# Kernel tuning notes

Measured on AMD Instinct MI355X. Metric: run time of the kernel, lower is better.

## Reference

```python
import jax, jax.numpy as jnp
import numpy as np

INPUT_SIZE = 128
HIDDEN_SIZE = 512
OUTPUT_SIZE = 128
NUM_LAYERS = 2
BATCH = 256
SEQ_LEN = 512

def _xavier(key, shape):
    fan_out, fan_in = shape
    limit = jnp.sqrt(6.0 / (fan_in + fan_out))
    return jax.random.uniform(key, shape, jnp.float32, -limit, limit)

def setup_inputs() -> dict:
    key = jax.random.key(0)
    ks = jax.random.split(key, 8)
    x = jax.random.normal(ks[0], (BATCH, SEQ_LEN, INPUT_SIZE), jnp.float32)
    hidden = jnp.zeros((NUM_LAYERS, BATCH, HIDDEN_SIZE), jnp.float32)
    W_ih0 = _xavier(ks[1], (HIDDEN_SIZE, INPUT_SIZE))
    W_hh0 = _xavier(ks[2], (HIDDEN_SIZE, HIDDEN_SIZE))
    W_ih1 = _xavier(ks[3], (HIDDEN_SIZE, HIDDEN_SIZE))
    W_hh1 = _xavier(ks[4], (HIDDEN_SIZE, HIDDEN_SIZE))
    b_ih0 = jnp.zeros((HIDDEN_SIZE,), jnp.float32)
    b_hh0 = jnp.zeros((HIDDEN_SIZE,), jnp.float32)
    b_ih1 = jnp.zeros((HIDDEN_SIZE,), jnp.float32)
    b_hh1 = jnp.zeros((HIDDEN_SIZE,), jnp.float32)
    fc_W = _xavier(ks[5], (OUTPUT_SIZE, HIDDEN_SIZE))
    fc_b = jnp.zeros((OUTPUT_SIZE,), jnp.float32)
    return {"x": x, "hidden": hidden,
            "W_ih0": W_ih0, "b_ih0": b_ih0, "W_hh0": W_hh0, "b_hh0": b_hh0,
            "W_ih1": W_ih1, "b_ih1": b_ih1, "W_hh1": W_hh1, "b_hh1": b_hh1,
            "fc_W": fc_W, "fc_b": fc_b}

def _run_layer(seq_tbi, h0, W_ih, b_ih, W_hh, b_hh):
    # seq_tbi: [T, B, I]; h0: [B, H]
    # Precompute input projection for all timesteps (one big GEMM).
    xin = jnp.einsum('tbi,hi->tbh', seq_tbi, W_ih) + b_ih + b_hh  # [T, B, H]
    def step(h, xt):
        h = jnp.tanh(xt + h @ W_hh.T)
        return h, h
    h_last, outs = jax.lax.scan(step, h0, xin)
    return h_last, outs  # outs: [T, B, H]

def reference(x, hidden, W_ih0, b_ih0, W_hh0, b_hh0, W_ih1, b_ih1, W_hh1, b_hh1, fc_W, fc_b):
    seq = jnp.transpose(x, (1, 0, 2))  # [T, B, I]
    h0_last, out0 = _run_layer(seq, hidden[0], W_ih0, b_ih0, W_hh0, b_hh0)
    h1_last, out1 = _run_layer(out0, hidden[1], W_ih1, b_ih1, W_hh1, b_hh1)
    new_hidden = jnp.stack([h0_last, h1_last], axis=0)  # [L, B, H]
    last_hidden = out1[-1]  # [B, H]
    output = last_hidden @ fc_W.T + fc_b  # [B, O]
    return output, new_hidden
```

## Files before the change

kernel.cpp:

```cpp
#include <hip/hip_runtime.h>

#define NB 256
#define NT 512
#define NI 128
#define NH 512
#define NO 128
#define NGRP 16
#define RPG 16
#define BPG 8

typedef __attribute__((ext_vector_type(8))) __bf16 bf16x8;
typedef __attribute__((ext_vector_type(4))) float  f32x4;
typedef unsigned long long u64;

#define MFMA16(a,b,c) __builtin_amdgcn_mfma_f32_16x16x32_bf16((a),(b),(c),0,0,0)

#define XSZ   (RPG*NI*2)
#define HSZ   (RPG*NH*2)
#define XOFF  0
#define H0OFF (2*XSZ)
#define H1OFF (H0OFF + HSZ)
#define SMEM_BYTES (H1OFF + HSZ)

#define SLABU   2048
#define TAGBASE 131072

__device__ __forceinline__ float fast_tanh(float x){
  x = fminf(15.f, fmaxf(-15.f, x));
  float e = __expf(2.f * x);
  return 1.f - 2.f / (e + 1.f);
}

__device__ __forceinline__ bf16x8 cvt8(float4 a, float4 b){
  bf16x8 r;
  r[0]=(__bf16)a.x; r[1]=(__bf16)a.y; r[2]=(__bf16)a.z; r[3]=(__bf16)a.w;
  r[4]=(__bf16)b.x; r[5]=(__bf16)b.y; r[6]=(__bf16)b.z; r[7]=(__bf16)b.w;
  return r;
}

__device__ __forceinline__ bf16x8 loadWfrag(const float* __restrict__ W, int ldk, int row, int k0){
  const float4* p = (const float4*)(W + (size_t)row * ldk + k0);
  return cvt8(p[0], p[1]);
}

__device__ __forceinline__ void st_u64(u64* p, u64 v){
  __hip_atomic_store(p, v, __ATOMIC_RELAXED, __HIP_MEMORY_SCOPE_AGENT);
}
__device__ __forceinline__ u64 ld_u64(const u64* p){
  return __hip_atomic_load(p, __ATOMIC_RELAXED, __HIP_MEMORY_SCOPE_AGENT);
}

__device__ __forceinline__ u64 pack4bf(f32x4 v){
  union { __bf16 h[4]; u64 u; } un;
  un.h[0]=(__bf16)v[0]; un.h[1]=(__bf16)v[1]; un.h[2]=(__bf16)v[2]; un.h[3]=(__bf16)v[3];
  return un.u;
}

__device__ __forceinline__ unsigned cksum(unsigned tick, u64 d){
  return tick + (unsigned)d + (unsigned)(d >> 32);
}

__device__ __forceinline__ u64* slab(u64* b, int l, int p, int g){
  return b + ((size_t)(((l << 1) | p) * NGRP + g)) * SLABU;
}

__global__ __launch_bounds__(256, 1)
void rnn_persistent(const float* __restrict__ x,
                    const float* __restrict__ hid,
                    const float* __restrict__ Wih0, const float* __restrict__ bih0,
                    const float* __restrict__ Whh0, const float* __restrict__ bhh0,
                    const float* __restrict__ Wih1, const float* __restrict__ bih1,
                    const float* __restrict__ Whh1, const float* __restrict__ bhh1,
                    const float* __restrict__ fcW,  const float* __restrict__ fcb,
                    float* __restrict__ out,
                    u64* __restrict__ ex)
{
  __shared__ __align__(16) char smem[SMEM_BYTES];

  const int tid  = threadIdx.x;
  const int lane = tid & 63;
  const int wv   = tid >> 6;
  const int lr   = lane & 15;
  const int lq   = lane >> 4;

  const int bq  = blockIdx.x;
  const int j   = (bq >> 3) & 7;
  const int g   = (bq & 7) + 8 * (bq >> 6);
  const int cb  = j * 64 + wv * 16;
  const int row0 = g * RPG;
  const int myq  = j * 16 + wv * 4 + lq;

  u64* const dat = ex;
  u64* const tag = ex + TAGBASE;

  bf16x8 wih0[4], whh0[16], wih1[16], whh1[16];
#pragma unroll
  for (int kt = 0; kt < 4;  ++kt) wih0[kt] = loadWfrag(Wih0, NI, cb + lr, kt*32 + lq*8);
#pragma unroll
  for (int kt = 0; kt < 16; ++kt) whh0[kt] = loadWfrag(Whh0, NH, cb + lr, kt*32 + lq*8);
#pragma unroll
  for (int kt = 0; kt < 16; ++kt) wih1[kt] = loadWfrag(Wih1, NH, cb + lr, kt*32 + lq*8);
#pragma unroll
  for (int kt = 0; kt < 16; ++kt) whh1[kt] = loadWfrag(Whh1, NH, cb + lr, kt*32 + lq*8);

  const f32x4 bias0 = *(const f32x4*)(bih0 + cb + lq*4) + *(const f32x4*)(bhh0 + cb + lq*4);
  const f32x4 bias1 = *(const f32x4*)(bih1 + cb + lq*4) + *(const f32x4*)(bhh1 + cb + lq*4);

  {
    int r = tid >> 4, i0 = (tid & 15) * 8;
    const float4* xp = (const float4*)(x + ((size_t)(row0 + r) * NT + 0) * NI + i0);
    bf16x8 v = cvt8(xp[0], xp[1]);
    int o = r * 256 + i0 * 2;
    *(bf16x8*)(smem + XOFF + (o ^ ((r & 7) << 4))) = v;
  }
#pragma unroll
  for (int it = 0; it < 4; ++it) {
    int e = it * 2048 + tid * 8;
    int r = e >> 9, c = e & 511;
    int o = r * 1024 + c * 2;
    const float4* hp0 = (const float4*)(hid + (size_t)(row0 + r) * NH + c);
    *(bf16x8*)(smem + H0OFF + (o ^ ((r & 7) << 4))) = cvt8(hp0[0], hp0[1]);
    const float4* hp1 = (const float4*)(hid + (size_t)NB * NH + (size_t)(row0 + r) * NH + c);
    *(bf16x8*)(smem + H1OFF + (o ^ ((r & 7) << 4))) = cvt8(hp1[0], hp1[1]);
  }
  __syncthreads();

#define HFRAG(base, kt) (*(const bf16x8*)((base) + lr * 1024 + (((kt) * 64 + lq * 16) ^ ((lr & 7) << 4))))

#define INGEST(V, D, T, TICK)                                                        \
  for (;;) {                                                                         \
    u64 tg_[8];                                                                      \
    _Pragma("unroll") for (int i_ = 0; i_ < 8; ++i_) V[i_]  = ld_u64((D) + i_*256 + tid); \
    _Pragma("unroll") for (int i_ = 0; i_ < 8; ++i_) tg_[i_] = ld_u64((T) + i_*256 + tid); \
    bool ok_ = true;                                                                 \
    _Pragma("unroll") for (int i_ = 0; i_ < 8; ++i_)                                 \
      ok_ &= ((unsigned)tg_[i_] == cksum((TICK), V[i_]));                            \
    if (ok_) break;                                                                  \
  }

  for (int t = 0; t <= NT; ++t) {
    const char* xA  = smem + XOFF + (t & 1) * XSZ;
    char* h0L = smem + H0OFF;
    char* h1L = smem + H1OFF;
    const bool do0 = (t < NT), do1 = (t > 0);
    const unsigned tick = (unsigned)(t + 1);

    u64* D0 = slab(dat, 0, t & 1, g);        u64* T0 = slab(tag, 0, t & 1, g);
    u64* D1 = slab(dat, 1, (t + 1) & 1, g);  u64* T1 = slab(tag, 1, (t + 1) & 1, g);

    if (do0) {
      f32x4 a0={0.f,0.f,0.f,0.f}, a1={0.f,0.f,0.f,0.f};
#pragma unroll
      for (int kt = 0; kt < 4; ++kt) {
        bf16x8 a = *(const bf16x8*)(xA + lr * 256 + ((kt * 64 + lq * 16) ^ ((lr & 7) << 4)));
        a0 = MFMA16(wih0[kt], a, a0);
      }
#pragma unroll
      for (int kt = 0; kt < 16; ++kt) {
        bf16x8 a = HFRAG(h0L, kt);
        if (kt & 1) a1 = MFMA16(whh0[kt], a, a1); else a0 = MFMA16(whh0[kt], a, a0);
      }
      f32x4 s = a0 + a1 + bias0;
      f32x4 h; h[0]=fast_tanh(s[0]); h[1]=fast_tanh(s[1]); h[2]=fast_tanh(s[2]); h[3]=fast_tanh(s[3]);
      if (t == NT - 1)
        *(f32x4*)(out + NB * NO + (size_t)(row0 + lr) * NH + cb + lq * 4) = h;
      u64 d = pack4bf(h);
      int idx = lr * 128 + myq;
      st_u64(D0 + idx, d);
      st_u64(T0 + idx, (u64)cksum(tick, d));
    }

    if (do1) {
      f32x4 c0={0.f,0.f,0.f,0.f}, c1={0.f,0.f,0.f,0.f};
#pragma unroll
      for (int kt = 0; kt < 16; ++kt) {
        bf16x8 a = HFRAG(h0L, kt);
        if (kt & 1) c1 = MFMA16(wih1[kt], a, c1); else c0 = MFMA16(wih1[kt], a, c0);
      }
#pragma unroll
      for (int kt = 0; kt < 16; ++kt) {
        bf16x8 a = HFRAG(h1L, kt);
        if (kt & 1) c1 = MFMA16(whh1[kt], a, c1); else c0 = MFMA16(whh1[kt], a, c0);
      }
      f32x4 s = c0 + c1 + bias1;
      f32x4 h; h[0]=fast_tanh(s[0]); h[1]=fast_tanh(s[1]); h[2]=fast_tanh(s[2]); h[3]=fast_tanh(s[3]);
      if (t == NT)
        *(f32x4*)(out + NB * NO + (size_t)NB * NH + (size_t)(row0 + lr) * NH + cb + lq * 4) = h;
      u64 d = pack4bf(h);
      int idx = lr * 128 + myq;
      st_u64(D1 + idx, d);
      st_u64(T1 + idx, (u64)cksum(tick, d));
    }
    asm volatile("" ::: "memory");
    if (t == NT) break;

    float4 xr0, xr1;
    const bool xpf = (t + 1 < NT);
    if (xpf) {
      int r = tid >> 4, i0 = (tid & 15) * 8;
      const float4* xp = (const float4*)(x + ((size_t)(row0 + r) * NT + (t + 1)) * NI + i0);
      xr0 = xp[0]; xr1 = xp[1];
    }

    u64 v0[8], v1[8];
    INGEST(v0, D0, T0, tick);
    if (do1) { INGEST(v1, D1, T1, tick); }

    __syncthreads();
#pragma unroll
    for (int it = 0; it < 8; ++it) {
      int o = (it * 256 + tid) * 8, r = o >> 10;
      *(u64*)(h0L + (o ^ ((r & 7) << 4))) = v0[it];
    }
    if (do1) {
#pragma unroll
      for (int it = 0; it < 8; ++it) {
        int o = (it * 256 + tid) * 8, r = o >> 10;
        *(u64*)(h1L + (o ^ ((r & 7) << 4))) = v1[it];
      }
    }
    if (xpf) {
      int r = tid >> 4, i0 = (tid & 15) * 8;
      bf16x8 v = cvt8(xr0, xr1);
      char* dst = smem + XOFF + ((t + 1) & 1) * XSZ;
      *(bf16x8*)(dst + ((r * 256 + i0 * 2) ^ ((r & 7) << 4))) = v;
    }
    __syncthreads();
  }

  {
    u64* DF = slab(dat, 1, 1, g);
    u64* TF = slab(tag, 1, 1, g);
    u64 vf[8];
    INGEST(vf, DF, TF, (unsigned)(NT + 1));
    __syncthreads();
    char* h1L = smem + H1OFF;
#pragma unroll
    for (int it = 0; it < 8; ++it) {
      int o = (it * 256 + tid) * 8, r = o >> 10;
      *(u64*)(h1L + (o ^ ((r & 7) << 4))) = vf[it];
    }
    __syncthreads();
  }
  if (wv == 0) {
    const char* h1L = smem + H1OFF;
    f32x4 acc = {0.f,0.f,0.f,0.f};
#pragma unroll
    for (int kt = 0; kt < 16; ++kt) {
      bf16x8 b = HFRAG(h1L, kt);
      bf16x8 a = loadWfrag(fcW, NH, j * 16 + lr, kt * 32 + lq * 8);
      acc = MFMA16(a, b, acc);
    }
    f32x4 fb = *(const f32x4*)(fcb + j * 16 + lq * 4);
    *(f32x4*)(out + (size_t)(row0 + lr) * NO + j * 16 + lq * 4) = acc + fb;
  }
#undef INGEST
#undef HFRAG
}

extern "C" void kernel_launch(void* const* d_in, const int* in_sizes, int n_in,
                              void* d_out, int out_size, void* d_ws, size_t ws_size,
                              hipStream_t stream)
{
  const float* x    = (const float*)d_in[0];
  const float* hid  = (const float*)d_in[1];
  const float* Wih0 = (const float*)d_in[2];
  const float* bih0 = (const float*)d_in[3];
  const float* Whh0 = (const float*)d_in[4];
  const float* bhh0 = (const float*)d_in[5];
  const float* Wih1 = (const float*)d_in[6];
  const float* bih1 = (const float*)d_in[7];
  const float* Whh1 = (const float*)d_in[8];
  const float* bhh1 = (const float*)d_in[9];
  const float* fcW  = (const float*)d_in[10];
  const float* fcb  = (const float*)d_in[11];
  float* out = (float*)d_out;

  u64* ex = (u64*)d_ws;

  (void)hipMemsetAsync(d_ws, 0, (size_t)2 * TAGBASE * sizeof(u64) == 0 ? 0 : (size_t)2 * 1024 * 1024, stream);

  hipLaunchKernelGGL(rnn_persistent, dim3(NGRP * BPG), dim3(256), 0, stream,
                     x, hid, Wih0, bih0, Whh0, bhh0, Wih1, bih1, Whh1, bhh1,
                     fcW, fcb, out, ex);
}
```

Measured before the change: 2.176 ms.

## Double-buffer hidden state in LDS and issue exchange loads right after stores

Hidden-state LDS buffers for both layers are double-buffered by timestep parity, which removes one of the two per-step block barriers. The per-step exchange loads from the global slab are issued right after each layer's own store, so polling overlaps the other layer's compute. Tags shrink from 64-bit to 32-bit words, which reduces exchange traffic and the memset size. In exchange, LDS use grows and the first poll may often miss and retry.

```diff
diff --git a/kernel.cpp b/kernel.cpp
--- a/kernel.cpp
+++ b/kernel.cpp
@@ -19,11 +19,11 @@
 #define HSZ   (RPG*NH*2)
 #define XOFF  0
 #define H0OFF (2*XSZ)
-#define H1OFF (H0OFF + HSZ)
-#define SMEM_BYTES (H1OFF + HSZ)
+#define H1OFF (H0OFF + 2*HSZ)
+#define SMEM_BYTES (H1OFF + 2*HSZ)
 
 #define SLABU   2048
-#define TAGBASE 131072
+#define DATAU   (4*NGRP*SLABU)
 
 __device__ __forceinline__ float fast_tanh(float x){
   x = fminf(15.f, fmaxf(-15.f, x));
@@ -49,6 +49,12 @@
 __device__ __forceinline__ u64 ld_u64(const u64* p){
   return __hip_atomic_load(p, __ATOMIC_RELAXED, __HIP_MEMORY_SCOPE_AGENT);
 }
+__device__ __forceinline__ void st_u32(unsigned* p, unsigned v){
+  __hip_atomic_store(p, v, __ATOMIC_RELAXED, __HIP_MEMORY_SCOPE_AGENT);
+}
+__device__ __forceinline__ unsigned ld_u32(const unsigned* p){
+  return __hip_atomic_load(p, __ATOMIC_RELAXED, __HIP_MEMORY_SCOPE_AGENT);
+}
 
 __device__ __forceinline__ u64 pack4bf(f32x4 v){
   union { __bf16 h[4]; u64 u; } un;
@@ -60,7 +66,10 @@
   return tick + (unsigned)d + (unsigned)(d >> 32);
 }
 
-__device__ __forceinline__ u64* slab(u64* b, int l, int p, int g){
+__device__ __forceinline__ u64* slabD(u64* b, int l, int p, int g){
+  return b + ((size_t)(((l << 1) | p) * NGRP + g)) * SLABU;
+}
+__device__ __forceinline__ unsigned* slabT(unsigned* b, int l, int p, int g){
   return b + ((size_t)(((l << 1) | p) * NGRP + g)) * SLABU;
 }
 
@@ -89,9 +98,10 @@
   const int cb  = j * 64 + wv * 16;
   const int row0 = g * RPG;
   const int myq  = j * 16 + wv * 4 + lq;
+  const int idx  = lr * 128 + myq;
 
   u64* const dat = ex;
-  u64* const tag = ex + TAGBASE;
+  unsigned* const tag = (unsigned*)(ex + DATAU);
 
   bf16x8 wih0[4], whh0[16], wih1[16], whh1[16];
 #pragma unroll
@@ -121,32 +131,42 @@
     const float4* hp0 = (const float4*)(hid + (size_t)(row0 + r) * NH + c);
     *(bf16x8*)(smem + H0OFF + (o ^ ((r & 7) << 4))) = cvt8(hp0[0], hp0[1]);
     const float4* hp1 = (const float4*)(hid + (size_t)NB * NH + (size_t)(row0 + r) * NH + c);
-    *(bf16x8*)(smem + H1OFF + (o ^ ((r & 7) << 4))) = cvt8(hp1[0], hp1[1]);
+    *(bf16x8*)(smem + H1OFF + HSZ + (o ^ ((r & 7) << 4))) = cvt8(hp1[0], hp1[1]);
   }
   __syncthreads();
 
 #define HFRAG(base, kt) (*(const bf16x8*)((base) + lr * 1024 + (((kt) * 64 + lq * 16) ^ ((lr & 7) << 4))))
 
-#define INGEST(V, D, T, TICK)                                                        \
-  for (;;) {                                                                         \
-    u64 tg_[8];                                                                      \
-    _Pragma("unroll") for (int i_ = 0; i_ < 8; ++i_) V[i_]  = ld_u64((D) + i_*256 + tid); \
-    _Pragma("unroll") for (int i_ = 0; i_ < 8; ++i_) tg_[i_] = ld_u64((T) + i_*256 + tid); \
-    bool ok_ = true;                                                                 \
+#define LOAD8(V, G, D, T)                                                            \
+  { _Pragma("unroll") for (int i_ = 0; i_ < 8; ++i_) V[i_] = ld_u64((D) + i_*256 + tid); \
+    _Pragma("unroll") for (int i_ = 0; i_ < 8; ++i_) G[i_] = ld_u32((T) + i_*256 + tid); }
+
+#define CHECK8(OK, V, G, TICK)                                                       \
+  { OK = true;                                                                       \
     _Pragma("unroll") for (int i_ = 0; i_ < 8; ++i_)                                 \
-      ok_ &= ((unsigned)tg_[i_] == cksum((TICK), V[i_]));                            \
-    if (ok_) break;                                                                  \
-  }
+      OK &= (G[i_] == cksum((TICK), V[i_])); }
+
+#define RESTAGE8(BASE, V)                                                            \
+  { _Pragma("unroll") for (int i_ = 0; i_ < 8; ++i_) {                               \
+      int o_ = (i_ * 256 + tid) * 8, r_ = o_ >> 10;                                  \
+      *(u64*)((BASE) + (o_ ^ ((r_ & 7) << 4))) = V[i_]; } }
 
   for (int t = 0; t <= NT; ++t) {
-    const char* xA  = smem + XOFF + (t & 1) * XSZ;
-    char* h0L = smem + H0OFF;
-    char* h1L = smem + H1OFF;
+    const char* xA  = smem + XOFF  + (t & 1) * XSZ;
+    const char* h0A = smem + H0OFF + (t & 1) * HSZ;
+    const char* h1A = smem + H1OFF + (t & 1) * HSZ;
+    char* h0N = smem + H0OFF + ((t + 1) & 1) * HSZ;
+    char* h1N = smem + H1OFF + ((t + 1) & 1) * HSZ;
     const bool do0 = (t < NT), do1 = (t > 0);
     const unsigned tick = (unsigned)(t + 1);
 
-    u64* D0 = slab(dat, 0, t & 1, g);        u64* T0 = slab(tag, 0, t & 1, g);
-    u64* D1 = slab(dat, 1, (t + 1) & 1, g);  u64* T1 = slab(tag, 1, (t + 1) & 1, g);
+    u64*      D0 = slabD(dat, 0, t & 1, g);
+    unsigned* T0 = slabT(tag, 0, t & 1, g);
+    u64*      D1 = slabD(dat, 1, (t + 1) & 1, g);
+    unsigned* T1 = slabT(tag, 1, (t + 1) & 1, g);
+
+    u64 v0[8], v1[8];
+    unsigned g0[8], g1[8];
 
     if (do0) {
       f32x4 a0={0.f,0.f,0.f,0.f}, a1={0.f,0.f,0.f,0.f};
@@ -157,7 +177,7 @@
       }
 #pragma unroll
       for (int kt = 0; kt < 16; ++kt) {
-        bf16x8 a = HFRAG(h0L, kt);
+        bf16x8 a = HFRAG(h0A, kt);
         if (kt & 1) a1 = MFMA16(whh0[kt], a, a1); else a0 = MFMA16(whh0[kt], a, a0);
       }
       f32x4 s = a0 + a1 + bias0;
@@ -165,21 +185,21 @@
       if (t == NT - 1)
         *(f32x4*)(out + NB * NO + (size_t)(row0 + lr) * NH + cb + lq * 4) = h;
       u64 d = pack4bf(h);
-      int idx = lr * 128 + myq;
       st_u64(D0 + idx, d);
-      st_u64(T0 + idx, (u64)cksum(tick, d));
+      st_u32(T0 + idx, cksum(tick, d));
+      LOAD8(v0, g0, D0, T0);
     }
 
     if (do1) {
       f32x4 c0={0.f,0.f,0.f,0.f}, c1={0.f,0.f,0.f,0.f};
 #pragma unroll
       for (int kt = 0; kt < 16; ++kt) {
-        bf16x8 a = HFRAG(h0L, kt);
+        bf16x8 a = HFRAG(h0A, kt);
         if (kt & 1) c1 = MFMA16(wih1[kt], a, c1); else c0 = MFMA16(wih1[kt], a, c0);
       }
 #pragma unroll
       for (int kt = 0; kt < 16; ++kt) {
-        bf16x8 a = HFRAG(h1L, kt);
+        bf16x8 a = HFRAG(h1A, kt);
         if (kt & 1) c1 = MFMA16(whh1[kt], a, c1); else c0 = MFMA16(whh1[kt], a, c0);
       }
       f32x4 s = c0 + c1 + bias1;
@@ -187,11 +207,10 @@
       if (t == NT)
         *(f32x4*)(out + NB * NO + (size_t)NB * NH + (size_t)(row0 + lr) * NH + cb + lq * 4) = h;
       u64 d = pack4bf(h);
-      int idx = lr * 128 + myq;
       st_u64(D1 + idx, d);
-      st_u64(T1 + idx, (u64)cksum(tick, d));
-    }
-    asm volatile("" ::: "memory");
+      st_u32(T1 + idx, cksum(tick, d));
+      LOAD8(v1, g1, D1, T1);
+    }
     if (t == NT) break;
 
     float4 xr0, xr1;
@@ -202,23 +221,18 @@
       xr0 = xp[0]; xr1 = xp[1];
     }
 
-    u64 v0[8], v1[8];
-    INGEST(v0, D0, T0, tick);
-    if (do1) { INGEST(v1, D1, T1, tick); }
-
-    __syncthreads();
-#pragma unroll
-    for (int it = 0; it < 8; ++it) {
-      int o = (it * 256 + tid) * 8, r = o >> 10;
-      *(u64*)(h0L + (o ^ ((r & 7) << 4))) = v0[it];
-    }
+    {
+      bool ok; CHECK8(ok, v0, g0, tick);
+      while (!ok) { LOAD8(v0, g0, D0, T0); CHECK8(ok, v0, g0, tick); }
+    }
+    RESTAGE8(h0N, v0);
+
     if (do1) {
-#pragma unroll
-      for (int it = 0; it < 8; ++it) {
-        int o = (it * 256 + tid) * 8, r = o >> 10;
-        *(u64*)(h1L + (o ^ ((r & 7) << 4))) = v1[it];
-      }
-    }
+      bool ok; CHECK8(ok, v1, g1, tick);
+      while (!ok) { LOAD8(v1, g1, D1, T1); CHECK8(ok, v1, g1, tick); }
+      RESTAGE8(h1N, v1);
+    }
+
     if (xpf) {
       int r = tid >> 4, i0 = (tid & 15) * 8;
       bf16x8 v = cvt8(xr0, xr1);
@@ -229,32 +243,34 @@
   }
 
   {
-    u64* DF = slab(dat, 1, 1, g);
-    u64* TF = slab(tag, 1, 1, g);
-    u64 vf[8];
-    INGEST(vf, DF, TF, (unsigned)(NT + 1));
+    u64*      DF = slabD(dat, 1, 1, g);
+    unsigned* TF = slabT(tag, 1, 1, g);
+    u64 vf[8]; unsigned gf[8];
+#pragma unroll
+    for (int i_ = 0; i_ < 8; ++i_) { vf[i_] = 0; gf[i_] = 0; }
+    bool ok = false;
+    LOAD8(vf, gf, DF, TF);
+    CHECK8(ok, vf, gf, (unsigned)(NT + 1));
+    while (!ok) { LOAD8(vf, gf, DF, TF); CHECK8(ok, vf, gf, (unsigned)(NT + 1)); }
+    char* hF = smem + H1OFF + HSZ;
+    RESTAGE8(hF, vf);
     __syncthreads();
-    char* h1L = smem + H1OFF;
-#pragma unroll
-    for (int it = 0; it < 8; ++it) {
-      int o = (it * 256 + tid) * 8, r = o >> 10;
-      *(u64*)(h1L + (o ^ ((r & 7) << 4))) = vf[it];
-    }
-    __syncthreads();
   }
   if (wv == 0) {
-    const char* h1L = smem + H1OFF;
+    const char* hF = smem + H1OFF + HSZ;
     f32x4 acc = {0.f,0.f,0.f,0.f};
 #pragma unroll
     for (int kt = 0; kt < 16; ++kt) {
-      bf16x8 b = HFRAG(h1L, kt);
+      bf16x8 b = HFRAG(hF, kt);
       bf16x8 a = loadWfrag(fcW, NH, j * 16 + lr, kt * 32 + lq * 8);
       acc = MFMA16(a, b, acc);
     }
     f32x4 fb = *(const f32x4*)(fcb + j * 16 + lq * 4);
     *(f32x4*)(out + (size_t)(row0 + lr) * NO + j * 16 + lq * 4) = acc + fb;
   }
-#undef INGEST
+#undef RESTAGE8
+#undef CHECK8
+#undef LOAD8
 #undef HFRAG
 }
 
@@ -278,7 +294,7 @@
 
   u64* ex = (u64*)d_ws;
 
-  (void)hipMemsetAsync(d_ws, 0, (size_t)2 * TAGBASE * sizeof(u64) == 0 ? 0 : (size_t)2 * 1024 * 1024, stream);
+  (void)hipMemsetAsync(d_ws, 0, (size_t)(1024 + 512) * 1024, stream);
 
   hipLaunchKernelGGL(rnn_persistent, dim3(NGRP * BPG), dim3(256), 0, stream,
                      x, hid, Wih0, bih0, Whh0, bhh0, Wih1, bih1, Whh1, bhh1,
```

Result: slower. 4.818 ms (+121.4%).
